# Performance work log

Measured on AMD Instinct MI355X. Metric: run time of the kernel, lower is better.

The kernel has to match this reference:

```python
import jax, jax.numpy as jnp
import numpy as np

L = 4          # decoder layers (model_config "[4,[0],0]")
D = 1024       # d_model
H = 16         # n_head
DH = 64        # d_head
DI = 4096      # d_inner
V = 16000      # n_token (add_eot=False)
S = 1024       # seq len
B = 4          # batch
EPS = 1e-5


def _layer_norm(x, g, b):
    mu = jnp.mean(x, axis=-1, keepdims=True)
    var = jnp.mean(jnp.square(x - mu), axis=-1, keepdims=True)
    return (x - mu) * jax.lax.rsqrt(var + EPS) * g + b


def _rel_shift(x):
    # x: [b, n, q, k]
    b, n, q, k = x.shape
    zero_pad = jnp.zeros((b, n, q, 1), dtype=x.dtype)
    xp = jnp.concatenate([zero_pad, x], axis=3)        # [b,n,q,k+1]
    xp = xp.reshape(b, n, k + 1, q)
    return xp[:, :, 1:, :].reshape(b, n, q, k)


def setup_inputs() -> dict:
    key = jax.random.key(0)
    ks = list(jax.random.split(key, 24))
    sd = 0.02
    inp = {}
    inp["tokens"] = jax.random.randint(ks[0], (S, B), 0, V)
    inp["word_emb"] = jax.random.normal(ks[1], (V, D), jnp.float32) * sd
    inp["r_w_bias"] = jax.random.normal(ks[2], (H, DH), jnp.float32) * sd
    inp["r_r_bias"] = jax.random.normal(ks[3], (H, DH), jnp.float32) * sd
    inp["qkv_w"] = jax.random.normal(ks[4], (L, D, 3 * H * DH), jnp.float32) * sd
    inp["qkv_b"] = jnp.zeros((L, 3 * H * DH), jnp.float32)
    inp["r_kw"] = jax.random.normal(ks[5], (L, D, H * DH), jnp.float32) * sd
    inp["r_kb"] = jnp.zeros((L, H * DH), jnp.float32)
    inp["o_w"] = jax.random.normal(ks[6], (L, H * DH, D), jnp.float32) * sd
    inp["o_b"] = jnp.zeros((L, D), jnp.float32)
    inp["ln1_g"] = jnp.ones((L, D), jnp.float32)
    inp["ln1_b"] = jnp.zeros((L, D), jnp.float32)
    inp["ff1_w"] = jax.random.normal(ks[7], (L, D, DI), jnp.float32) * sd
    inp["ff1_b"] = jnp.zeros((L, DI), jnp.float32)
    inp["ff2_w"] = jax.random.normal(ks[8], (L, DI, D), jnp.float32) * sd
    inp["ff2_b"] = jnp.zeros((L, D), jnp.float32)
    inp["ln2_g"] = jnp.ones((L, D), jnp.float32)
    inp["ln2_b"] = jnp.zeros((L, D), jnp.float32)
    inp["final_w"] = jax.random.normal(ks[9], (D, V), jnp.float32) * sd
    inp["final_b"] = jnp.zeros((V,), jnp.float32)
    return inp


def reference(tokens, word_emb, r_w_bias, r_r_bias, qkv_w, qkv_b, r_kw, r_kb,
              o_w, o_b, ln1_g, ln1_b, ff1_w, ff1_b, ff2_w, ff2_b,
              ln2_g, ln2_b, final_w, final_b):
    s, b = tokens.shape
    h = word_emb[tokens]                                 # [S,B,D]
    # sinusoidal relative positions, pos_seq = klen-1 ... 0
    pos_seq = jnp.arange(s - 1, -1, -1, dtype=h.dtype)
    inv_freq = 1.0 / (10000.0 ** (jnp.arange(0, D, 2, dtype=h.dtype) / D))
    sinu = pos_seq[:, None] * inv_freq[None, :]
    r = jnp.concatenate([jnp.sin(sinu), jnp.cos(sinu)], axis=-1)   # [S,D]
    # causal mask: True = masked (j > i)
    mask = jnp.triu(jnp.ones((s, s), dtype=bool), k=1)
    scale = 1.0 / (DH ** 0.5)
    neg_inf = jnp.asarray(-jnp.inf, dtype=h.dtype)

    for l in range(L):
        qkv = h @ qkv_w[l] + qkv_b[l]                    # [S,B,3*H*DH]
        q, k, v = jnp.split(qkv, 3, axis=-1)
        q = q.reshape(s, b, H, DH)
        k = k.reshape(s, b, H, DH)
        v = v.reshape(s, b, H, DH)
        rk = (r @ r_kw[l] + r_kb[l]).reshape(s, H, DH)   # [S,H,DH]
        AC = jnp.einsum('ibnd,jbnd->bnij', q + r_w_bias, k)
        BD = jnp.einsum('ibnd,jnd->bnij', q + r_r_bias, rk)
        BD = _rel_shift(BD)
        score = scale * (AC + BD)
        score = jnp.where(mask[None, None, :, :], neg_inf, score)
        prob = jax.nn.softmax(score, axis=-1)
        vec = jnp.einsum('bnij,jbnd->ibnd', prob, v).reshape(s, b, H * DH)
        attn_out = vec @ o_w[l] + o_b[l]
        h = _layer_norm(h + attn_out, ln1_g[l], ln1_b[l])
        ff = jax.nn.gelu(h @ ff1_w[l] + ff1_b[l], approximate=False) @ ff2_w[l] + ff2_b[l]
        h = _layer_norm(h + ff, ln2_g[l], ln2_b[l])

    logits = h @ final_w + final_b                       # [S,B,V]
    return logits
```

## Files before the change

kernel.cpp:

```cpp
#include <hip/hip_runtime.h>

#define S 1024
#define Bb 4
#define Hh 16
#define DHh 64
#define Dm 1024
#define DIi 4096
#define Vv 16000
#define Lll 4

typedef __attribute__((ext_vector_type(4))) float f32x4;
typedef __attribute__((ext_vector_type(8))) __bf16 bf16x8;
typedef __attribute__((ext_vector_type(8))) unsigned short u16x8;
typedef __attribute__((ext_vector_type(4))) unsigned short u16x4;

__device__ __forceinline__ unsigned short f2bf(float f) {
  unsigned int u = __float_as_uint(f);
  u += 0x7fffu + ((u >> 16) & 1u);
  return (unsigned short)(u >> 16);
}
__device__ __forceinline__ float bf2f(unsigned short u) {
  return __uint_as_float(((unsigned int)u) << 16);
}

__device__ __forceinline__ void gload_lds16(const void* g, void* l) {
  __builtin_amdgcn_global_load_lds((const __attribute__((address_space(1))) unsigned int*)g,
                                   (__attribute__((address_space(3))) unsigned int*)l, 16, 0, 0);
}

__device__ __forceinline__ f32x4 mfma_bf16(bf16x8 a, bf16x8 b, f32x4 c) {
  return __builtin_amdgcn_mfma_f32_16x16x32_bf16(a, b, c, 0, 0, 0);
}

__global__ __launch_bounds__(256) void embed_k(const int* __restrict__ tokens,
                                               const float* __restrict__ we,
                                               float* __restrict__ h,
                                               unsigned short* __restrict__ hb) {
  int row = blockIdx.x;
  int t = threadIdx.x;
  int tok = tokens[row];
  f32x4 v = *(const f32x4*)&we[(long)tok * Dm + t * 4];
  *(f32x4*)&h[(long)row * Dm + t * 4] = v;
  u16x4 r;
#pragma unroll
  for (int e = 0; e < 4; ++e) r[e] = f2bf(v[e]);
  *(u16x4*)&hb[(long)row * Dm + t * 4] = r;
}

__global__ __launch_bounds__(256) void posr_k(unsigned short* __restrict__ r) {
  int idx = blockIdx.x * 256 + threadIdx.x;
  int u = idx >> 10, d = idx & 1023;
  float pos = (float)(S - 1 - u);
  int j = d & 511;
  float invf = powf(10000.0f, -(float)j * (1.0f / 512.0f));
  float a = pos * invf;
  r[idx] = f2bf(d < 512 ? sinf(a) : cosf(a));
}

__global__ __launch_bounds__(256) void wcvt_t(const float* __restrict__ W,
                                              unsigned short* __restrict__ WT,
                                              int Kd, int Nd) {
  __shared__ unsigned short tile[32][40];
  int n0 = blockIdx.x * 32, k0 = blockIdx.y * 32;
  const bool inb = n0 < Nd;
  const float* Wb = W + (long)blockIdx.z * Kd * Nd;
  unsigned short* WTb = WT + (long)blockIdx.z * Kd * Nd;
  int t = threadIdx.x;
  int rr = t >> 3, c4 = (t & 7) * 4;
  f32x4 v = {0.f, 0.f, 0.f, 0.f};
  if (inb) v = *(const f32x4*)&Wb[(long)(k0 + rr) * Nd + n0 + c4];
#pragma unroll
  for (int e = 0; e < 4; ++e) tile[rr][c4 + e] = f2bf(v[e]);
  __syncthreads();
  if (t < 128) {
    int n = t >> 2, k8 = (t & 3) * 8;
    u16x8 pk;
#pragma unroll
    for (int e = 0; e < 8; ++e) pk[e] = tile[k8 + e][n];
    *(u16x8*)&WTb[(long)(n0 + n) * Kd + k0 + k8] = pk;
  }
}

template <int EPI>
__global__ __launch_bounds__(512, 2) void gemm256(const unsigned short* __restrict__ A,
                                                  const unsigned short* __restrict__ BT,
                                                  const float* __restrict__ bias,
                                                  void* __restrict__ Cout,
                                                  int M, int N, int K,
                                                  int ntm, int ntn, int morder) {
  __shared__ unsigned short lds[65536];
  unsigned short* Al = lds;
  unsigned short* Bl = lds + 32768;
  const int tid = threadIdx.x, lane = tid & 63, w = tid >> 6;
  const int la = lane & 15, hi = lane >> 4;
  const int nwg = gridDim.x;
  const int qq = nwg >> 3, rr = nwg & 7;
  const int xcd = blockIdx.x & 7, loc = blockIdx.x >> 3;
  const int wg = (xcd < rr ? xcd * (qq + 1) : rr * (qq + 1) + (xcd - rr) * qq) + loc;
  int bm, bn;
  if (morder) { bm = (wg % ntm) * 256; bn = (wg / ntm) * 256; }
  else        { bn = (wg % ntn) * 256; bm = (wg / ntn) * 256; }
  const int wr = w >> 2, wc = w & 3;
  f32x4 acc[8][4] = {};

  const unsigned short* ag = A + (long)(bm + w * 16 + la) * K + hi * 8;
  const unsigned short* bg = BT + (long)(bn + w * 16 + la) * K + hi * 8;
  unsigned short* Asg = Al + w * 512;
  unsigned short* Bsg = Bl + w * 512;
  const unsigned short* Ard = Al + wr * 4096 + lane * 8;
  const unsigned short* Brd = Bl + wc * 2048 + lane * 8;
  const int NT = K >> 5;

#define STAGE(t) { \
    long ko_ = (long)(t) * 32; int bo_ = ((t) & 3) * 8192; \
    gload_lds16(ag + ko_, Asg + bo_); \
    gload_lds16(ag + ko_ + (long)128 * K, Asg + bo_ + 4096); \
    gload_lds16(bg + ko_, Bsg + bo_); \
    gload_lds16(bg + ko_ + (long)128 * K, Bsg + bo_ + 4096); }

#define COMPUTE(t) { \
    const int bo_ = ((t) & 3) * 8192; \
    bf16x8 af[8], bq[4]; \
    _Pragma("unroll") \
    for (int m = 0; m < 8; ++m) af[m] = *(const bf16x8*)(Ard + bo_ + m * 512); \
    _Pragma("unroll") \
    for (int n = 0; n < 4; ++n) bq[n] = *(const bf16x8*)(Brd + bo_ + n * 512); \
    __builtin_amdgcn_s_setprio(1); \
    _Pragma("unroll") \
    for (int m = 0; m < 8; ++m) \
      _Pragma("unroll") \
      for (int n = 0; n < 4; ++n) acc[m][n] = mfma_bf16(af[m], bq[n], acc[m][n]); \
    __builtin_amdgcn_s_setprio(0); }

  STAGE(0); STAGE(1); STAGE(2);
  int t = 0;
  for (; t < NT - 3; ++t) {
    asm volatile("s_waitcnt vmcnt(8)" ::: "memory");
    __builtin_amdgcn_s_barrier();
    __builtin_amdgcn_sched_barrier(0);
    STAGE(t + 3);
    COMPUTE(t);
  }
  asm volatile("s_waitcnt vmcnt(8)" ::: "memory");
  __builtin_amdgcn_s_barrier();
  __builtin_amdgcn_sched_barrier(0);
  COMPUTE(t); ++t;
  asm volatile("s_waitcnt vmcnt(4)" ::: "memory");
  __builtin_amdgcn_s_barrier();
  __builtin_amdgcn_sched_barrier(0);
  COMPUTE(t); ++t;
  asm volatile("s_waitcnt vmcnt(0)" ::: "memory");
  __builtin_amdgcn_s_barrier();
  __builtin_amdgcn_sched_barrier(0);
  COMPUTE(t);
#undef STAGE
#undef COMPUTE

#pragma unroll
  for (int m = 0; m < 8; ++m) {
#pragma unroll
    for (int n = 0; n < 4; ++n) {
      int col = bn + wc * 64 + n * 16 + la;
      if (col < N) {
        float bv = bias[col];
        int row = bm + wr * 128 + m * 16 + hi * 4;
#pragma unroll
        for (int e = 0; e < 4; ++e) {
          float v = acc[m][n][e] + bv;
          if (EPI == 0) {
            ((float*)Cout)[(long)(row + e) * N + col] = v;
          } else if (EPI == 1) {
            ((unsigned short*)Cout)[(long)(row + e) * N + col] = f2bf(v);
          } else {
            float g = 0.5f * v * (1.0f + erff(v * 0.70710678118f));
            ((unsigned short*)Cout)[(long)(row + e) * N + col] = f2bf(g);
          }
        }
      }
    }
  }
}

template <int EPI>
__global__ __launch_bounds__(256) void gemm_bt(const unsigned short* __restrict__ A,
                                               const unsigned short* __restrict__ BT,
                                               const float* __restrict__ bias,
                                               void* __restrict__ Cout,
                                               int M, int N, int K, int ntn) {
  __shared__ unsigned short As[128 * 64];
  __shared__ unsigned short Bs[128 * 64];
  const int tid = threadIdx.x;
  const int lane = tid & 63;
  const int w = tid >> 6;
  const int nwg = gridDim.x;
  const int qq = nwg >> 3, rr = nwg & 7;
  const int xcd = blockIdx.x & 7, loc = blockIdx.x >> 3;
  const int wg = (xcd < rr ? xcd * (qq + 1) : rr * (qq + 1) + (xcd - rr) * qq) + loc;
  const int bn = (wg % ntn) * 128, bm = (wg / ntn) * 128;
  const int wr = (w >> 1) * 64, wc = (w & 1) * 64;
  const int la = lane & 15, hi = lane >> 4;
  f32x4 acc[4][4] = {};

  const int rrow = tid >> 3;
  const int rcol = ((tid & 7) ^ (rrow & 7)) * 8;
  const unsigned short* ag = A + (long)(bm + rrow) * K + rcol;
  const unsigned short* bg = BT + (long)(bn + rrow) * K + rcol;
  const int las = la & 7;
  const int ro0 = (hi ^ las) * 8;
  const int ro1 = ((hi + 4) ^ las) * 8;

  for (int k0 = 0; k0 < K; k0 += 64) {
    __syncthreads();
#pragma unroll
    for (int c = 0; c < 4; ++c) {
      gload_lds16(ag + (long)c * 32 * K + k0, &As[c * 2048 + w * 512]);
      gload_lds16(bg + (long)c * 32 * K + k0, &Bs[c * 2048 + w * 512]);
    }
    __syncthreads();
#pragma unroll
    for (int kk = 0; kk < 2; ++kk) {
      const int ro = kk ? ro1 : ro0;
      bf16x8 af[4], bq[4];
#pragma unroll
      for (int mi = 0; mi < 4; ++mi)
        af[mi] = *(const bf16x8*)&As[(wr + mi * 16 + la) * 64 + ro];
#pragma unroll
      for (int ni = 0; ni < 4; ++ni)
        bq[ni] = *(const bf16x8*)&Bs[(wc + ni * 16 + la) * 64 + ro];
#pragma unroll
      for (int mi = 0; mi < 4; ++mi)
#pragma unroll
        for (int ni = 0; ni < 4; ++ni)
          acc[mi][ni] = mfma_bf16(af[mi], bq[ni], acc[mi][ni]);
    }
  }
  const int cr = hi * 4;
#pragma unroll
  for (int mi = 0; mi < 4; ++mi) {
#pragma unroll
    for (int ni = 0; ni < 4; ++ni) {
      int col = bn + wc + ni * 16 + la;
      float bv = bias[col];
      int row = bm + wr + mi * 16 + cr;
#pragma unroll
      for (int e = 0; e < 4; ++e) {
        float v = acc[mi][ni][e] + bv;
        if (EPI == 0) {
          ((float*)Cout)[(long)(row + e) * N + col] = v;
        } else if (EPI == 1) {
          ((unsigned short*)Cout)[(long)(row + e) * N + col] = f2bf(v);
        } else {
          float g = 0.5f * v * (1.0f + erff(v * 0.70710678118f));
          ((unsigned short*)Cout)[(long)(row + e) * N + col] = f2bf(g);
        }
      }
    }
  }
}

template <int EPI>
__global__ __launch_bounds__(256) void gemm_bt64(const unsigned short* __restrict__ A,
                                                 const unsigned short* __restrict__ BT,
                                                 const float* __restrict__ bias,
                                                 void* __restrict__ Cout,
                                                 int M, int N, int K, int ntn) {
  __shared__ unsigned short As[64 * 64];
  __shared__ unsigned short Bs[128 * 64];
  const int tid = threadIdx.x;
  const int lane = tid & 63;
  const int w = tid >> 6;
  const int nwg = gridDim.x;
  const int qq = nwg >> 3, rr = nwg & 7;
  const int xcd = blockIdx.x & 7, loc = blockIdx.x >> 3;
  const int wg = (xcd < rr ? xcd * (qq + 1) : rr * (qq + 1) + (xcd - rr) * qq) + loc;
  const int bn = (wg % ntn) * 128, bm = (wg / ntn) * 64;
  const int wr = (w >> 1) * 32, wc = (w & 1) * 64;
  const int la = lane & 15, hi = lane >> 4;
  f32x4 acc[2][4] = {};

  const int rrow = tid >> 3;
  const int rcol = ((tid & 7) ^ (rrow & 7)) * 8;
  const unsigned short* ag = A + (long)(bm + rrow) * K + rcol;
  const unsigned short* bg = BT + (long)(bn + rrow) * K + rcol;
  const int las = la & 7;
  const int ro0 = (hi ^ las) * 8;
  const int ro1 = ((hi + 4) ^ las) * 8;

  for (int k0 = 0; k0 < K; k0 += 64) {
    __syncthreads();
#pragma unroll
    for (int c = 0; c < 2; ++c)
      gload_lds16(ag + (long)c * 32 * K + k0, &As[c * 2048 + w * 512]);
#pragma unroll
    for (int c = 0; c < 4; ++c)
      gload_lds16(bg + (long)c * 32 * K + k0, &Bs[c * 2048 + w * 512]);
    __syncthreads();
#pragma unroll
    for (int kk = 0; kk < 2; ++kk) {
      const int ro = kk ? ro1 : ro0;
      bf16x8 af[2], bq[4];
#pragma unroll
      for (int mi = 0; mi < 2; ++mi)
        af[mi] = *(const bf16x8*)&As[(wr + mi * 16 + la) * 64 + ro];
#pragma unroll
      for (int ni = 0; ni < 4; ++ni)
        bq[ni] = *(const bf16x8*)&Bs[(wc + ni * 16 + la) * 64 + ro];
#pragma unroll
      for (int mi = 0; mi < 2; ++mi)
#pragma unroll
        for (int ni = 0; ni < 4; ++ni)
          acc[mi][ni] = mfma_bf16(af[mi], bq[ni], acc[mi][ni]);
    }
  }
  const int cr = hi * 4;
#pragma unroll
  for (int mi = 0; mi < 2; ++mi) {
#pragma unroll
    for (int ni = 0; ni < 4; ++ni) {
      int col = bn + wc + ni * 16 + la;
      float bv = bias[col];
      int row = bm + wr + mi * 16 + cr;
#pragma unroll
      for (int e = 0; e < 4; ++e) {
        float v = acc[mi][ni][e] + bv;
        if (EPI == 0) {
          ((float*)Cout)[(long)(row + e) * N + col] = v;
        } else if (EPI == 1) {
          ((unsigned short*)Cout)[(long)(row + e) * N + col] = f2bf(v);
        } else {
          float g = 0.5f * v * (1.0f + erff(v * 0.70710678118f));
          ((unsigned short*)Cout)[(long)(row + e) * N + col] = f2bf(g);
        }
      }
    }
  }
}

__global__ __launch_bounds__(256) void qkv_prep(const unsigned short* __restrict__ q3,
                                                const float* __restrict__ rwb,
                                                const float* __restrict__ rrb,
                                                unsigned short* __restrict__ qw,
                                                unsigned short* __restrict__ qr,
                                                unsigned short* __restrict__ kb) {
  int idx = blockIdx.x * 256 + threadIdx.x;
  int c8 = (idx & 127) * 8;
  int row = idx >> 7;
  int s = row >> 2, b = row & 3;
  int n = c8 >> 6, d = c8 & 63;
  u16x8 qv = *(const u16x8*)&q3[(long)row * 3072 + c8];
  u16x8 kv = *(const u16x8*)&q3[(long)row * 3072 + 1024 + c8];
  long o = ((long)(b * Hh + n) * S + s) * 64 + d;
  u16x8 ow, orr;
#pragma unroll
  for (int e = 0; e < 8; ++e) {
    float q = bf2f(qv[e]);
    ow[e] = f2bf(q + rwb[c8 + e]);
    orr[e] = f2bf(q + rrb[c8 + e]);
  }
  *(u16x8*)&qw[o] = ow;
  *(u16x8*)&qr[o] = orr;
  *(u16x8*)&kb[o] = kv;
}

__global__ __launch_bounds__(256) void vt_prep(const unsigned short* __restrict__ q3,
                                               unsigned short* __restrict__ vT) {
  __shared__ unsigned short tile[64][72];
  const int it = blockIdx.x, bn = blockIdx.y;
  const int nh = bn & 15, bbv = bn >> 4;
  const int t = threadIdx.x;
  const int i0 = t >> 3, c8 = (t & 7) * 8;
#pragma unroll
  for (int c = 0; c < 2; ++c) {
    int i = i0 + c * 32;
    u16x8 v = *(const u16x8*)&q3[((long)(it * 64 + i) * Bb + bbv) * 3072 + 2048 + nh * 64 + c8];
    *(u16x8*)&tile[i][c8] = v;
  }
  __syncthreads();
  for (int cc = t; cc < 512; cc += 256) {
    int d = cc >> 3, i8 = (cc & 7) * 8;
    u16x8 pk;
#pragma unroll
    for (int e = 0; e < 8; ++e) pk[e] = tile[i8 + e][d];
    *(u16x8*)&vT[((long)bn * 64 + d) * S + it * 64 + i8] = pk;
  }
}

__global__ __launch_bounds__(256) void rkb_prep(const unsigned short* __restrict__ rkall,
                                                unsigned short* __restrict__ rkb) {
  int idx = blockIdx.x * 256 + threadIdx.x;
  int d8 = (idx & 7) * 8;
  int u = (idx >> 3) & 1023;
  int nl = idx >> 13;
  int l = nl >> 4, n = nl & 15;
  u16x8 v = *(const u16x8*)&rkall[(long)u * 4096 + l * 1024 + n * 64 + d8];
  *(u16x8*)&rkb[(long)idx * 8] = v;
}

__global__ __launch_bounds__(256) void attn_k(const unsigned short* __restrict__ qw,
                                              const unsigned short* __restrict__ qr,
                                              const unsigned short* __restrict__ kbuf,
                                              const unsigned short* __restrict__ vT,
                                              const unsigned short* __restrict__ rk,
                                              unsigned short* __restrict__ vec) {
  __shared__ unsigned short Ks[2][64 * 64];
  __shared__ unsigned short Vs[2][64 * 64];
  __shared__ unsigned short plds[4][16][72];
  const int tid = threadIdx.x, lane = tid & 63, w = tid >> 6;
  const int bn = blockIdx.x & 63;
  const int it = 15 - (blockIdx.x >> 6);
  const int nh = bn & 15, bbv = bn >> 4;
  const int la = lane & 15, hi = lane >> 4, lk = hi * 8;
  const int hi4 = hi * 4;
  const unsigned short* kbase = kbuf + (long)bn * S * 64;
  const unsigned short* vbase = vT + (long)bn * 64 * S;
  const unsigned short* rbase = rk + (long)nh * S * 64;

  const int q0 = w * 128 + lane;
  const int r0 = q0 >> 3, c0s = (q0 & 7) ^ (r0 & 7);
  const int q1 = q0 + 64;
  const int r1 = q1 >> 3, c1s = (q1 & 7) ^ (r1 & 7);

  const int iw = it * 64 + w * 16;
  bf16x8 qwf[2], qrf[2];
  {
    const unsigned short* qp = qw + ((long)bn * S + iw + la) * 64 + lk;
    qwf[0] = *(const bf16x8*)qp;
    qwf[1] = *(const bf16x8*)(qp + 32);
    const unsigned short* qp2 = qr + ((long)bn * S + iw + la) * 64 + lk;
    qrf[0] = *(const bf16x8*)qp2;
    qrf[1] = *(const bf16x8*)(qp2 + 32);
  }
  f32x4 opv[4] = {};
  float m_ = -3e38f;
  float l_[4] = {0.f, 0.f, 0.f, 0.f};
  int cur = 0;

  gload_lds16(kbase + (long)r0 * 64 + c0s * 8, &Ks[cur][w * 1024]);
  gload_lds16(kbase + (long)r1 * 64 + c1s * 8, &Ks[cur][w * 1024 + 512]);
  gload_lds16(vbase + (long)r0 * S + c0s * 8, &Vs[cur][w * 1024]);
  gload_lds16(vbase + (long)r1 * S + c1s * 8, &Vs[cur][w * 1024 + 512]);
  __syncthreads();

  for (int jt = 0; jt <= it; ++jt) {
    const int j0 = jt * 64;
    const bool edge = (jt == it);
    if (jt < it) {
      const int jn = j0 + 64;
      gload_lds16(kbase + (long)(jn + r0) * 64 + c0s * 8, &Ks[cur ^ 1][w * 1024]);
      gload_lds16(kbase + (long)(jn + r1) * 64 + c1s * 8, &Ks[cur ^ 1][w * 1024 + 512]);
      gload_lds16(vbase + (long)r0 * S + jn + c0s * 8, &Vs[cur ^ 1][w * 1024]);
      gload_lds16(vbase + (long)r1 * S + jn + c1s * 8, &Vs[cur ^ 1][w * 1024 + 512]);
    }
    const int u0 = S - 16 - iw + j0;
    bf16x8 rf[10];
#pragma unroll
    for (int g = 0; g < 5; ++g) {
      int u = u0 + g * 16 + la;
      if (edge) u = (u > S - 1) ? (S - 1) : u;
      const unsigned short* rp = rbase + (long)u * 64 + lk;
      rf[2 * g] = *(const bf16x8*)rp;
      rf[2 * g + 1] = *(const bf16x8*)(rp + 32);
    }
    f32x4 ac[4] = {};
#pragma unroll
    for (int f = 0; f < 4; ++f) {
      int row = f * 16 + la;
      const unsigned short* kl = &Ks[cur][row * 64];
      bf16x8 k0 = *(const bf16x8*)(kl + (((hi) ^ (row & 7)) << 3));
      bf16x8 k1 = *(const bf16x8*)(kl + (((hi + 4) ^ (row & 7)) << 3));
      ac[f] = mfma_bf16(qwf[0], k0, ac[f]);
      ac[f] = mfma_bf16(qwf[1], k1, ac[f]);
    }
    f32x4 gg[5] = {};
#pragma unroll
    for (int g = 0; g < 5; ++g) {
      gg[g] = mfma_bf16(qrf[0], rf[2 * g], gg[g]);
      gg[g] = mfma_bf16(qrf[1], rf[2 * g + 1], gg[g]);
    }
    float p[4][4];
#pragma unroll
    for (int f = 0; f < 4; ++f) {
#pragma unroll
      for (int e = 0; e < 4; ++e) {
        int r = hi4 + e;
        float x = (la >= 15 - r) ? gg[f][e] : gg[f + 1][e];
        int src = (lane & 48) | ((la + 15 - r) & 15);
        float bd = __shfl(x, src, 64);
        float sc = (ac[f][e] + bd) * 0.125f;
        if (edge) {
          int i_ = iw + r, j_ = j0 + f * 16 + la;
          sc = (j_ > i_) ? -1e30f : sc;
        }
        p[f][e] = sc;
      }
    }
    float mx = p[0][0];
#pragma unroll
    for (int f = 0; f < 4; ++f)
#pragma unroll
      for (int e = 0; e < 4; ++e) mx = fmaxf(mx, p[f][e]);
#pragma unroll
    for (int o = 1; o < 16; o <<= 1) mx = fmaxf(mx, __shfl_xor(mx, o, 64));
    if (!__all(mx <= m_ + 8.0f)) {
      float mnew = fmaxf(m_, mx);
      float alpha = __expf(m_ - mnew);
      m_ = mnew;
#pragma unroll
      for (int e = 0; e < 4; ++e) l_[e] *= alpha;
#pragma unroll
      for (int d = 0; d < 4; ++d)
#pragma unroll
        for (int e = 0; e < 4; ++e) opv[d][e] *= alpha;
    }
#pragma unroll
    for (int e = 0; e < 4; ++e) {
      float rs = 0.f;
#pragma unroll
      for (int f = 0; f < 4; ++f) {
        p[f][e] = __expf(p[f][e] - m_);
        rs += p[f][e];
      }
      l_[e] += rs;
    }
#pragma unroll
    for (int f = 0; f < 4; ++f)
#pragma unroll
      for (int e = 0; e < 4; ++e)
        plds[w][hi4 + e][f * 16 + la] = f2bf(p[f][e]);
    bf16x8 pa0 = *(const bf16x8*)&plds[w][la][lk];
    bf16x8 pa1 = *(const bf16x8*)&plds[w][la][32 + lk];
#pragma unroll
    for (int d = 0; d < 4; ++d) {
      int dd = d * 16 + la;
      const unsigned short* vl = &Vs[cur][dd * 64];
      bf16x8 v0 = *(const bf16x8*)(vl + (((hi) ^ (dd & 7)) << 3));
      bf16x8 v1 = *(const bf16x8*)(vl + (((hi + 4) ^ (dd & 7)) << 3));
      opv[d] = mfma_bf16(pa0, v0, opv[d]);
      opv[d] = mfma_bf16(pa1, v1, opv[d]);
    }
    __syncthreads();
    if (jt < it) cur ^= 1;
  }
#pragma unroll
  for (int e = 0; e < 4; ++e) {
#pragma unroll
    for (int o = 1; o < 16; o <<= 1) l_[e] += __shfl_xor(l_[e], o, 64);
  }
#pragma unroll
  for (int d = 0; d < 4; ++d) {
#pragma unroll
    for (int e = 0; e < 4; ++e) {
      int i_ = iw + hi4 + e;
      int col = nh * 64 + d * 16 + la;
      vec[((long)i_ * Bb + bbv) * 1024 + col] = f2bf(opv[d][e] / l_[e]);
    }
  }
}

__global__ __launch_bounds__(256) void add_ln(float* __restrict__ h, const float* __restrict__ x,
                                              const float* __restrict__ g, const float* __restrict__ b,
                                              unsigned short* __restrict__ hb) {
  __shared__ float red[8];
  int row = blockIdx.x, t = threadIdx.x;
  long base = (long)row * 1024 + t * 4;
  f32x4 hv = *(const f32x4*)&h[base];
  f32x4 xv = *(const f32x4*)&x[base];
  f32x4 y = hv + xv;
  float s = y[0] + y[1] + y[2] + y[3];
  float q = y[0] * y[0] + y[1] * y[1] + y[2] * y[2] + y[3] * y[3];
#pragma unroll
  for (int o = 1; o < 64; o <<= 1) {
    s += __shfl_xor(s, o, 64);
    q += __shfl_xor(q, o, 64);
  }
  int w = t >> 6, lane = t & 63;
  if (lane == 0) { red[w] = s; red[4 + w] = q; }
  __syncthreads();
  s = red[0] + red[1] + red[2] + red[3];
  q = red[4] + red[5] + red[6] + red[7];
  float mu = s * (1.0f / 1024.0f);
  float var = q * (1.0f / 1024.0f) - mu * mu;
  float rstd = rsqrtf(var + 1e-5f);
  f32x4 gv = *(const f32x4*)&g[t * 4];
  f32x4 bv = *(const f32x4*)&b[t * 4];
  f32x4 o;
  u16x4 ob;
#pragma unroll
  for (int e = 0; e < 4; ++e) {
    o[e] = (y[e] - mu) * rstd * gv[e] + bv[e];
    ob[e] = f2bf(o[e]);
  }
  *(f32x4*)&h[base] = o;
  *(u16x4*)&hb[base] = ob;
}

extern "C" void kernel_launch(void* const* d_in, const int* in_sizes, int n_in,
                              void* d_out, int out_size, void* d_ws, size_t ws_size,
                              hipStream_t stream) {
  const int* tokens = (const int*)d_in[0];
  const float* word_emb = (const float*)d_in[1];
  const float* rwb = (const float*)d_in[2];
  const float* rrb = (const float*)d_in[3];
  const float* qkv_w = (const float*)d_in[4];
  const float* qkv_b = (const float*)d_in[5];
  const float* r_kw = (const float*)d_in[6];
  const float* r_kb = (const float*)d_in[7];
  const float* o_w = (const float*)d_in[8];
  const float* o_b = (const float*)d_in[9];
  const float* ln1g = (const float*)d_in[10];
  const float* ln1b = (const float*)d_in[11];
  const float* ff1w = (const float*)d_in[12];
  const float* ff1b = (const float*)d_in[13];
  const float* ff2w = (const float*)d_in[14];
  const float* ff2b = (const float*)d_in[15];
  const float* ln2g = (const float*)d_in[16];
  const float* ln2b = (const float*)d_in[17];
  const float* fw = (const float*)d_in[18];
  const float* fb = (const float*)d_in[19];

  char* ws = (char*)d_ws;
  unsigned short* WBF = (unsigned short*)(ws);
  float* H = (float*)(ws + 33554432);
  unsigned short* HB = (unsigned short*)(ws + 50331648);
  unsigned short* GB = (unsigned short*)(ws + 58720256);
  unsigned short* RBF = (unsigned short*)(ws + 92274688);

  char* ob = (char*)d_out;
  float* OUTF = (float*)ob;
  unsigned short* OUTH = (unsigned short*)ob;
  unsigned short* QW = (unsigned short*)(ob + 67108864);
  unsigned short* QR = (unsigned short*)(ob + 75497472);
  unsigned short* KB = (unsigned short*)(ob + 83886080);
  unsigned short* VT = (unsigned short*)(ob + 92274688);
  unsigned short* RKB = (unsigned short*)(ob + 100663296);
  float* OUT = (float*)d_out;

  embed_k<<<4096, 256, 0, stream>>>(tokens, word_emb, H, HB);
  posr_k<<<4096, 256, 0, stream>>>(RBF);
  wcvt_t<<<dim3(32, 32, 4), 256, 0, stream>>>(r_kw, WBF, 1024, 1024);
  gemm_bt<1><<<256, 256, 0, stream>>>(RBF, WBF, r_kb, OUTH, 1024, 4096, 1024, 32);
  rkb_prep<<<2048, 256, 0, stream>>>(OUTH, RKB);

  for (int l = 0; l < Lll; ++l) {
    wcvt_t<<<dim3(96, 32, 1), 256, 0, stream>>>(qkv_w + (long)l * 1024 * 3072, WBF, 1024, 3072);
    gemm_bt<1><<<768, 256, 0, stream>>>(HB, WBF, qkv_b + l * 3072, OUTH, 4096, 3072, 1024, 24);
    qkv_prep<<<2048, 256, 0, stream>>>(OUTH, rwb, rrb, QW, QR, KB);
    vt_prep<<<dim3(16, 64), 256, 0, stream>>>(OUTH, VT);
    attn_k<<<1024, 256, 0, stream>>>(QW, QR, KB, VT, RKB + (long)l * Hh * S * 64, HB);
    wcvt_t<<<dim3(32, 32, 1), 256, 0, stream>>>(o_w + (long)l * 1024 * 1024, WBF, 1024, 1024);
    gemm_bt64<0><<<512, 256, 0, stream>>>(HB, WBF, o_b + l * 1024, OUTF, 4096, 1024, 1024, 8);
    add_ln<<<4096, 256, 0, stream>>>(H, OUTF, ln1g + l * 1024, ln1b + l * 1024, HB);

    wcvt_t<<<dim3(128, 32, 1), 256, 0, stream>>>(ff1w + (long)l * 1024 * 4096, WBF, 1024, 4096);
    gemm_bt<2><<<1024, 256, 0, stream>>>(HB, WBF, ff1b + l * 4096, GB, 4096, 4096, 1024, 32);
    wcvt_t<<<dim3(32, 128, 1), 256, 0, stream>>>(ff2w + (long)l * 4096 * 1024, WBF, 4096, 1024);
    gemm_bt64<0><<<512, 256, 0, stream>>>(GB, WBF, ff2b + l * 1024, OUTF, 4096, 1024, 4096, 8);
    add_ln<<<4096, 256, 0, stream>>>(H, OUTF, ln2g + l * 1024, ln2b + l * 1024, HB);
  }

  wcvt_t<<<dim3(504, 32, 1), 256, 0, stream>>>(fw, WBF, 1024, 16000);
  gemm256<0><<<1008, 512, 0, stream>>>(HB, WBF, fb, OUT, 4096, 16000, 1024, 16, 63, 1);
}
```

Measured before the change: 1.399 ms.

## Process 128-query tiles per attention block to share K/V LDS loads

The attention kernel now uses 512-thread blocks (8 waves) that each cover 128 query rows instead of 64, so every K/V tile staged in LDS serves twice as many queries and the grid is halved. Each thread loads one K and one V chunk per tile instead of two. Waves whose 16 rows lie entirely before a key tile skip its compute, and the causal mask is now applied per wave rather than only on the last tile. The cost is coarser causal load balance across blocks, idle waves on diagonal tiles, and a higher occupancy demand from launch_bounds(512,6).

Result: slower. 1.680 ms (+20.0%).

```diff
diff --git a/kernel.cpp b/kernel.cpp
--- a/kernel.cpp
+++ b/kernel.cpp
@@ -396,18 +396,19 @@
   *(u16x8*)&rkb[(long)idx * 8] = v;
 }
 
-__global__ __launch_bounds__(256) void attn_k(const unsigned short* __restrict__ qw,
-                                              const unsigned short* __restrict__ qr,
-                                              const unsigned short* __restrict__ kbuf,
-                                              const unsigned short* __restrict__ vT,
-                                              const unsigned short* __restrict__ rk,
-                                              unsigned short* __restrict__ vec) {
+__global__ __launch_bounds__(512, 6) void attn_k(const unsigned short* __restrict__ qw,
+                                                 const unsigned short* __restrict__ qr,
+                                                 const unsigned short* __restrict__ kbuf,
+                                                 const unsigned short* __restrict__ vT,
+                                                 const unsigned short* __restrict__ rk,
+                                                 unsigned short* __restrict__ vec) {
   __shared__ unsigned short Ks[2][64 * 64];
   __shared__ unsigned short Vs[2][64 * 64];
-  __shared__ unsigned short plds[4][16][72];
+  __shared__ unsigned short plds[8][16][72];
   const int tid = threadIdx.x, lane = tid & 63, w = tid >> 6;
   const int bn = blockIdx.x & 63;
-  const int it = 15 - (blockIdx.x >> 6);
+  const int qt = 7 - (blockIdx.x >> 6);
+  const int itmax = 2 * qt + 1;
   const int nh = bn & 15, bbv = bn >> 4;
   const int la = lane & 15, hi = lane >> 4, lk = hi * 8;
   const int hi4 = hi * 4;
@@ -415,12 +416,9 @@
   const unsigned short* vbase = vT + (long)bn * 64 * S;
   const unsigned short* rbase = rk + (long)nh * S * 64;
 
-  const int q0 = w * 128 + lane;
-  const int r0 = q0 >> 3, c0s = (q0 & 7) ^ (r0 & 7);
-  const int q1 = q0 + 64;
-  const int r1 = q1 >> 3, c1s = (q1 & 7) ^ (r1 & 7);
-
-  const int iw = it * 64 + w * 16;
+  const int r0 = tid >> 3, c0s = (tid & 7) ^ (r0 & 7);
+
+  const int iw = qt * 128 + w * 16;
   bf16x8 qwf[2], qrf[2];
   {
     const unsigned short* qp = qw + ((long)bn * S + iw + la) * 64 + lk;
@@ -435,111 +433,109 @@
   float l_[4] = {0.f, 0.f, 0.f, 0.f};
   int cur = 0;
 
-  gload_lds16(kbase + (long)r0 * 64 + c0s * 8, &Ks[cur][w * 1024]);
-  gload_lds16(kbase + (long)r1 * 64 + c1s * 8, &Ks[cur][w * 1024 + 512]);
-  gload_lds16(vbase + (long)r0 * S + c0s * 8, &Vs[cur][w * 1024]);
-  gload_lds16(vbase + (long)r1 * S + c1s * 8, &Vs[cur][w * 1024 + 512]);
+  gload_lds16(kbase + (long)r0 * 64 + c0s * 8, &Ks[0][w * 512]);
+  gload_lds16(vbase + (long)r0 * S + c0s * 8, &Vs[0][w * 512]);
   __syncthreads();
 
-  for (int jt = 0; jt <= it; ++jt) {
+  for (int jt = 0; jt <= itmax; ++jt) {
     const int j0 = jt * 64;
-    const bool edge = (jt == it);
-    if (jt < it) {
+    if (jt < itmax) {
       const int jn = j0 + 64;
-      gload_lds16(kbase + (long)(jn + r0) * 64 + c0s * 8, &Ks[cur ^ 1][w * 1024]);
-      gload_lds16(kbase + (long)(jn + r1) * 64 + c1s * 8, &Ks[cur ^ 1][w * 1024 + 512]);
-      gload_lds16(vbase + (long)r0 * S + jn + c0s * 8, &Vs[cur ^ 1][w * 1024]);
-      gload_lds16(vbase + (long)r1 * S + jn + c1s * 8, &Vs[cur ^ 1][w * 1024 + 512]);
-    }
-    const int u0 = S - 16 - iw + j0;
-    bf16x8 rf[10];
-#pragma unroll
-    for (int g = 0; g < 5; ++g) {
-      int u = u0 + g * 16 + la;
-      if (edge) u = (u > S - 1) ? (S - 1) : u;
-      const unsigned short* rp = rbase + (long)u * 64 + lk;
-      rf[2 * g] = *(const bf16x8*)rp;
-      rf[2 * g + 1] = *(const bf16x8*)(rp + 32);
-    }
-    f32x4 ac[4] = {};
-#pragma unroll
-    for (int f = 0; f < 4; ++f) {
-      int row = f * 16 + la;
-      const unsigned short* kl = &Ks[cur][row * 64];
-      bf16x8 k0 = *(const bf16x8*)(kl + (((hi) ^ (row & 7)) << 3));
-      bf16x8 k1 = *(const bf16x8*)(kl + (((hi + 4) ^ (row & 7)) << 3));
-      ac[f] = mfma_bf16(qwf[0], k0, ac[f]);
-      ac[f] = mfma_bf16(qwf[1], k1, ac[f]);
-    }
-    f32x4 gg[5] = {};
-#pragma unroll
-    for (int g = 0; g < 5; ++g) {
-      gg[g] = mfma_bf16(qrf[0], rf[2 * g], gg[g]);
-      gg[g] = mfma_bf16(qrf[1], rf[2 * g + 1], gg[g]);
-    }
-    float p[4][4];
-#pragma unroll
-    for (int f = 0; f < 4; ++f) {
+      gload_lds16(kbase + (long)(jn + r0) * 64 + c0s * 8, &Ks[cur ^ 1][w * 512]);
+      gload_lds16(vbase + (long)r0 * S + jn + c0s * 8, &Vs[cur ^ 1][w * 512]);
+    }
+    if (j0 <= iw + 15) {
+      const bool edge = (j0 + 63 > iw);
+      const int u0 = S - 16 - iw + j0;
+      bf16x8 rf[10];
+#pragma unroll
+      for (int g = 0; g < 5; ++g) {
+        int u = u0 + g * 16 + la;
+        u = (u > S - 1) ? (S - 1) : u;
+        const unsigned short* rp = rbase + (long)u * 64 + lk;
+        rf[2 * g] = *(const bf16x8*)rp;
+        rf[2 * g + 1] = *(const bf16x8*)(rp + 32);
+      }
+      f32x4 ac[4] = {};
+#pragma unroll
+      for (int f = 0; f < 4; ++f) {
+        int row = f * 16 + la;
+        const unsigned short* kl = &Ks[cur][row * 64];
+        bf16x8 k0 = *(const bf16x8*)(kl + (((hi) ^ (row & 7)) << 3));
+        bf16x8 k1 = *(const bf16x8*)(kl + (((hi + 4) ^ (row & 7)) << 3));
+        ac[f] = mfma_bf16(qwf[0], k0, ac[f]);
+        ac[f] = mfma_bf16(qwf[1], k1, ac[f]);
+      }
+      f32x4 gg[5] = {};
+#pragma unroll
+      for (int g = 0; g < 5; ++g) {
+        gg[g] = mfma_bf16(qrf[0], rf[2 * g], gg[g]);
+        gg[g] = mfma_bf16(qrf[1], rf[2 * g + 1], gg[g]);
+      }
+      float p[4][4];
+#pragma unroll
+      for (int f = 0; f < 4; ++f) {
+#pragma unroll
+        for (int e = 0; e < 4; ++e) {
+          int r = hi4 + e;
+          float x = (la >= 15 - r) ? gg[f][e] : gg[f + 1][e];
+          int src = (lane & 48) | ((la + 15 - r) & 15);
+          float bd = __shfl(x, src, 64);
+          float sc = (ac[f][e] + bd) * 0.125f;
+          if (edge) {
+            int i_ = iw + r, j_ = j0 + f * 16 + la;
+            sc = (j_ > i_) ? -1e30f : sc;
+          }
+          p[f][e] = sc;
+        }
+      }
+      float mx = p[0][0];
+#pragma unroll
+      for (int f = 0; f < 4; ++f)
+#pragma unroll
+        for (int e = 0; e < 4; ++e) mx = fmaxf(mx, p[f][e]);
+#pragma unroll
+      for (int o = 1; o < 16; o <<= 1) mx = fmaxf(mx, __shfl_xor(mx, o, 64));
+      if (!__all(mx <= m_ + 8.0f)) {
+        float mnew = fmaxf(m_, mx);
+        float alpha = __expf(m_ - mnew);
+        m_ = mnew;
+#pragma unroll
+        for (int e = 0; e < 4; ++e) l_[e] *= alpha;
+#pragma unroll
+        for (int d = 0; d < 4; ++d)
+#pragma unroll
+          for (int e = 0; e < 4; ++e) opv[d][e] *= alpha;
+      }
 #pragma unroll
       for (int e = 0; e < 4; ++e) {
-        int r = hi4 + e;
-        float x = (la >= 15 - r) ? gg[f][e] : gg[f + 1][e];
-        int src = (lane & 48) | ((la + 15 - r) & 15);
-        float bd = __shfl(x, src, 64);
-        float sc = (ac[f][e] + bd) * 0.125f;
-        if (edge) {
-          int i_ = iw + r, j_ = j0 + f * 16 + la;
-          sc = (j_ > i_) ? -1e30f : sc;
+        float rs = 0.f;
+#pragma unroll
+        for (int f = 0; f < 4; ++f) {
+          p[f][e] = __expf(p[f][e] - m_);
+          rs += p[f][e];
         }
-        p[f][e] = sc;
-      }
-    }
-    float mx = p[0][0];
-#pragma unroll
-    for (int f = 0; f < 4; ++f)
-#pragma unroll
-      for (int e = 0; e < 4; ++e) mx = fmaxf(mx, p[f][e]);
-#pragma unroll
-    for (int o = 1; o < 16; o <<= 1) mx = fmaxf(mx, __shfl_xor(mx, o, 64));
-    if (!__all(mx <= m_ + 8.0f)) {
-      float mnew = fmaxf(m_, mx);
-      float alpha = __expf(m_ - mnew);
-      m_ = mnew;
-#pragma unroll
-      for (int e = 0; e < 4; ++e) l_[e] *= alpha;
-#pragma unroll
-      for (int d = 0; d < 4; ++d)
-#pragma unroll
-        for (int e = 0; e < 4; ++e) opv[d][e] *= alpha;
-    }
-#pragma unroll
-    for (int e = 0; e < 4; ++e) {
-      float rs = 0.f;
-#pragma unroll
-      for (int f = 0; f < 4; ++f) {
-        p[f][e] = __expf(p[f][e] - m_);
-        rs += p[f][e];
-      }
-      l_[e] += rs;
-    }
-#pragma unroll
-    for (int f = 0; f < 4; ++f)
-#pragma unroll
-      for (int e = 0; e < 4; ++e)
-        plds[w][hi4 + e][f * 16 + la] = f2bf(p[f][e]);
-    bf16x8 pa0 = *(const bf16x8*)&plds[w][la][lk];
-    bf16x8 pa1 = *(const bf16x8*)&plds[w][la][32 + lk];
-#pragma unroll
-    for (int d = 0; d < 4; ++d) {
-      int dd = d * 16 + la;
-      const unsigned short* vl = &Vs[cur][dd * 64];
-      bf16x8 v0 = *(const bf16x8*)(vl + (((hi) ^ (dd & 7)) << 3));
-      bf16x8 v1 = *(const bf16x8*)(vl + (((hi + 4) ^ (dd & 7)) << 3));
-      opv[d] = mfma_bf16(pa0, v0, opv[d]);
-      opv[d] = mfma_bf16(pa1, v1, opv[d]);
+        l_[e] += rs;
+      }
+#pragma unroll
+      for (int f = 0; f < 4; ++f)
+#pragma unroll
+        for (int e = 0; e < 4; ++e)
+          plds[w][hi4 + e][f * 16 + la] = f2bf(p[f][e]);
+      bf16x8 pa0 = *(const bf16x8*)&plds[w][la][lk];
+      bf16x8 pa1 = *(const bf16x8*)&plds[w][la][32 + lk];
+#pragma unroll
+      for (int d = 0; d < 4; ++d) {
+        int dd = d * 16 + la;
+        const unsigned short* vl = &Vs[cur][dd * 64];
+        bf16x8 v0 = *(const bf16x8*)(vl + (((hi) ^ (dd & 7)) << 3));
+        bf16x8 v1 = *(const bf16x8*)(vl + (((hi + 4) ^ (dd & 7)) << 3));
+        opv[d] = mfma_bf16(pa0, v0, opv[d]);
+        opv[d] = mfma_bf16(pa1, v1, opv[d]);
+      }
     }
     __syncthreads();
-    if (jt < it) cur ^= 1;
+    if (jt < itmax) cur ^= 1;
   }
 #pragma unroll
   for (int e = 0; e < 4; ++e) {
@@ -646,7 +642,7 @@
     gemm_bt<1><<<768, 256, 0, stream>>>(HB, WBF, qkv_b + l * 3072, OUTH, 4096, 3072, 1024, 24);
     qkv_prep<<<2048, 256, 0, stream>>>(OUTH, rwb, rrb, QW, QR, KB);
     vt_prep<<<dim3(16, 64), 256, 0, stream>>>(OUTH, VT);
-    attn_k<<<1024, 256, 0, stream>>>(QW, QR, KB, VT, RKB + (long)l * Hh * S * 64, HB);
+    attn_k<<<512, 512, 0, stream>>>(QW, QR, KB, VT, RKB + (long)l * Hh * S * 64, HB);
     wcvt_t<<<dim3(32, 32, 1), 256, 0, stream>>>(o_w + (long)l * 1024 * 1024, WBF, 1024, 1024);
     gemm_bt64<0><<<512, 256, 0, stream>>>(HB, WBF, o_b + l * 1024, OUTF, 4096, 1024, 1024, 8);
     add_ln<<<4096, 256, 0, stream>>>(H, OUTF, ln1g + l * 1024, ln1b + l * 1024, HB);
```
